# Kernel tuning notes

Measured on AMD Instinct MI355X. Metric: run time of the kernel, lower is better.

The kernel has to match this reference:

```python
import jax, jax.numpy as jnp
import numpy as np

B_J0 = 0.01
BETA = 1.8
GAMMA = 0.5
LENS = 0.5
TAU_M = 20.0
DT = 1.0
IN_SIZE = 4
FULL_LEN = 784
T_STEPS = FULL_LEN // IN_SIZE  # 196 sequential steps
H1, H2, H3 = 512, 512, 512
OUT = 10
BATCH = 256


@jax.custom_vjp
def spike_fn(x):
    # ActFun_adp: heaviside forward, rectangular surrogate backward
    return (x > 0).astype(x.dtype)

def _spike_fwd(x):
    return (x > 0).astype(x.dtype), x

def _spike_bwd(x, g):
    return (GAMMA * g * (jnp.abs(x) < LENS).astype(g.dtype),)

spike_fn.defvjp(_spike_fwd, _spike_bwd)


def _make_mask(dim, c_min, c_max, min_dc, max_dc, phase_max, T=784):
    # Faithful port of create_general_mask
    dc_steps = np.linspace(min_dc, max_dc, dim)
    cycles = np.linspace(c_min, c_max, dim)
    phases = np.linspace(0.0, float(int(phase_max * c_max)), dim)
    rows = []
    for cyc, dc, ph in zip(cycles, dc_steps, phases):
        cyc = int(np.ceil(cyc))
        on = int(np.ceil(dc * cyc))
        pat = [1] * on + [0] * (cyc - on)
        p = int(np.round(ph))
        if p > 0:
            pat = pat[-p:] + pat[:-p]
        rows.append(pat * (T // cyc) + pat[: T % cyc])
    return jnp.asarray(np.array(rows, dtype=np.float32))


def setup_inputs() -> dict:
    key = jax.random.key(0)
    ks = jax.random.split(key, 8)

    def xav(k, o, i):
        return jax.random.normal(k, (o, i), jnp.float32) * np.float32(np.sqrt(2.0 / (o + i)))

    return {
        "x": jax.random.uniform(ks[0], (BATCH, FULL_LEN), jnp.float32),
        "W_i2h1": xav(ks[1], H1, IN_SIZE), "b_i2h1": jnp.zeros(H1, jnp.float32),
        "W_h2h1": xav(ks[2], H1, H1), "b_h2h1": jnp.zeros(H1, jnp.float32),
        "W_i2h2": xav(ks[3], H2, H1), "b_i2h2": jnp.zeros(H2, jnp.float32),
        "W_h2h2": xav(ks[4], H2, H2), "b_h2h2": jnp.zeros(H2, jnp.float32),
        "W_i2h3": xav(ks[5], H3, H2), "b_i2h3": jnp.zeros(H3, jnp.float32),
        "W_h2o": xav(ks[6], OUT, H3), "b_h2o": jnp.zeros(OUT, jnp.float32),
        "tau_adp_h1": jnp.full((H1,), 700.0, jnp.float32),
        "tau_adp_h2": jnp.full((H2,), 700.0, jnp.float32),
        "tau_adp_h3": jnp.full((H3,), 700.0, jnp.float32),
        "mask1": _make_mask(H1, 2, 10, 0.1, 0.9, 0.5),
        "mask2": _make_mask(H2, 2, 10, 0.1, 0.9, 0.5),
        "mask3": _make_mask(H3, 2, 10, 0.1, 0.9, 0.5),
    }


def _forward(x, params, mask1, mask2, mask3):
    (W_i2h1, b_i2h1, W_h2h1, b_h2h1, W_i2h2, b_i2h2, W_h2h2, b_h2h2,
     W_i2h3, b_i2h3, W_h2o, b_h2o, tau1, tau2, tau3) = params
    N = x.shape[0]
    # Faithful to torch: condition uses self.T (196), not 784, so most steps
    # reuse the last IN_SIZE columns.
    cols = np.stack([
        np.arange(s * IN_SIZE, s * IN_SIZE + IN_SIZE)
        if s * IN_SIZE < T_STEPS - IN_SIZE
        else np.arange(FULL_LEN - IN_SIZE, FULL_LEN)
        for s in range(T_STEPS)
    ])
    x_seq = jnp.transpose(x[:, cols], (1, 0, 2))  # (T, N, IN)
    alpha = jnp.exp(jnp.float32(-DT / TAU_M))
    ro1 = jnp.exp(-DT / tau1)
    ro2 = jnp.exp(-DT / tau2)
    ro3 = jnp.exp(-DT / tau3)
    m1_seq = mask1[:, :T_STEPS].T  # (T, H1)
    m2_seq = mask2[:, :T_STEPS].T
    m3_seq = mask3[:, :T_STEPS].T

    def upd(inputs, mem, spk, ro, b, mask):
        # mem_update_NU_adp_skip, isAdapt=1
        b = ro * b + (1.0 - ro) * spk
        Bth = B_J0 + BETA * b
        new_mem = mem * alpha + (1.0 - alpha) * inputs - Bth * spk * DT
        mem = jnp.where(mask == 0, mem, new_mem)
        spk = spike_fn(mem - Bth) * mask
        return mem, spk, b

    def step(carry, xs):
        mem1, s1, bb1, mem2, s2, bb2, mem3, s3, bb3, acc = carry
        x_t, mk1, mk2, mk3 = xs
        h1 = x_t @ W_i2h1.T + b_i2h1 + s1 @ W_h2h1.T + b_h2h1
        mem1, s1, bb1 = upd(h1, mem1, s1, ro1, bb1, mk1)
        h2 = s1 @ W_i2h2.T + b_i2h2 + s2 @ W_h2h2.T + b_h2h2
        mem2, s2, bb2 = upd(h2, mem2, s2, ro2, bb2, mk2)
        h3 = s2 @ W_i2h3.T + b_i2h3
        mem3, s3, bb3 = upd(h3, mem3, s3, ro3, bb3, mk3)
        acc = acc + s3 @ W_h2o.T + b_h2o
        return (mem1, s1, bb1, mem2, s2, bb2, mem3, s3, bb3, acc), None

    z = lambda h: jnp.zeros((N, h), x.dtype)
    bj = lambda h: jnp.full((N, h), B_J0, x.dtype)  # b starts at scalar b_j0
    carry0 = (z(H1), z(H1), bj(H1), z(H2), z(H2), bj(H2), z(H3), z(H3), bj(H3), z(OUT))
    carry, _ = jax.lax.scan(step, carry0, (x_seq, m1_seq, m2_seq, m3_seq))
    return carry[-1] / T_STEPS


def reference(x, W_i2h1, b_i2h1, W_h2h1, b_h2h1, W_i2h2, b_i2h2, W_h2h2, b_h2h2,
              W_i2h3, b_i2h3, W_h2o, b_h2o, tau_adp_h1, tau_adp_h2, tau_adp_h3,
              mask1, mask2, mask3):
    params = (W_i2h1, b_i2h1, W_h2h1, b_h2h1, W_i2h2, b_i2h2, W_h2h2, b_h2h2,
              W_i2h3, b_i2h3, W_h2o, b_h2o, tau_adp_h1, tau_adp_h2, tau_adp_h3)
    return _forward(x, params, mask1, mask2, mask3)
```

## Files before the change

kernel.cpp:

```cpp
#include <hip/hip_runtime.h>

#define H 512
#define TSTEPS 196
#define FLEN 784
#define NBATCH 256

typedef float f4 __attribute__((ext_vector_type(4)));
typedef unsigned long long ull;

#define SLOTB  1050624u
#define SLOTF  262656
#define PADOFF 1048576u
#define MBOFF_F 1050624

__global__ void transpose4(const float* __restrict__ a,
                           const float* __restrict__ b,
                           const float* __restrict__ c,
                           const float* __restrict__ d,
                           float* __restrict__ ws)
{
    __shared__ float tile[32][33];
    const float* src = (blockIdx.z == 0) ? a : (blockIdx.z == 1) ? b
                     : (blockIdx.z == 2) ? c : d;
    float* dst = ws + (size_t)blockIdx.z * SLOTF;
    int bx = blockIdx.x * 32, by = blockIdx.y * 32;
    int tx = threadIdx.x, ty = threadIdx.y;
    for (int r = ty; r < 32; r += 8)
        tile[r][tx] = src[(by + r) * H + bx + tx];
    __syncthreads();
    for (int r = ty; r < 32; r += 8)
        dst[(bx + r) * H + by + tx] = tile[tx][r];
}

__global__ void maskbits(const float* __restrict__ m1, const float* __restrict__ m2,
                         const float* __restrict__ m3, float* __restrict__ ws)
{
    int t = blockIdx.x;
    int z = blockIdx.y;
    int l = threadIdx.x;
    if (z == 3) {
        int idx = t * 64 + l;
        if (idx < 4 * 512) {
            int slot = idx >> 9, pos = idx & 511;
            ws[(size_t)slot * SLOTF + 512 * 512 + pos] = 0.0f;
        }
        return;
    }
    ull* mb = (ull*)(ws + MBOFF_F);
    const float* src = (z == 0) ? m1 : (z == 1) ? m2 : m3;
    for (int w = 0; w < 8; ++w) {
        ull bl = __ballot(src[(w * 64 + l) * FLEN + t] != 0.0f);
        if (l == 0) mb[(size_t)z * (TSTEPS * 8) + t * 8 + w] = bl;
    }
}

__device__ __forceinline__ f4 gsingle(const char* __restrict__ base,
                                      const unsigned* __restrict__ list,
                                      int lo, int hi, unsigned uoff)
{
    f4 a0 = (f4)0.0f, a1 = (f4)0.0f, a2 = (f4)0.0f, a3 = (f4)0.0f;
    for (int i = lo; i < hi; i += 4) {
        unsigned o0 = list[i]     + uoff;
        unsigned o1 = list[i + 1] + uoff;
        unsigned o2 = list[i + 2] + uoff;
        unsigned o3 = list[i + 3] + uoff;
        a0 += *(const f4*)(base + o0);
        a1 += *(const f4*)(base + o1);
        a2 += *(const f4*)(base + o2);
        a3 += *(const f4*)(base + o3);
    }
    return (a0 + a1) + (a2 + a3);
}

__device__ __forceinline__ float sum8(const float* __restrict__ p, int j)
{
    float s0 = p[j] + p[512 + j];
    float s1 = p[1024 + j] + p[1536 + j];
    float s2 = p[2048 + j] + p[2560 + j];
    float s3 = p[3072 + j] + p[3584 + j];
    return (s0 + s1) + (s2 + s3);
}

__device__ __forceinline__ float mbit(const ull* __restrict__ mb, int t, int j)
{
    return ((mb[t * 8 + (j >> 6)] >> (j & 63)) & 1ull) ? 1.0f : 0.0f;
}

__global__ __launch_bounds__(1024)
void lsnn_main(const float* __restrict__ x,
               const float* __restrict__ Wi1,
               const float* __restrict__ bi1, const float* __restrict__ bh1,
               const float* __restrict__ bi2, const float* __restrict__ bh2,
               const float* __restrict__ bi3,
               const float* __restrict__ Wo,  const float* __restrict__ bo,
               const float* __restrict__ tau1, const float* __restrict__ tau2,
               const float* __restrict__ tau3,
               const float* __restrict__ ws,
               float* __restrict__ out)
{
    const char* wsb  = (const char*)ws;
    const char* B_H1 = wsb;
    const char* B_I2 = wsb + SLOTB;
    const char* B_H2 = wsb + 2 * SLOTB;
    const char* B_I3 = wsb + 3 * SLOTB;
    const ull* mb1 = (const ull*)(ws + MBOFF_F);
    const ull* mb2 = mb1 + TSTEPS * 8;
    const ull* mb3 = mb2 + TSTEPS * 8;

    const int n    = blockIdx.x;
    const int tid  = threadIdx.x;
    const int lane = tid & 63;
    const bool lowh = tid < 512;
    const int j    = lowh ? tid : tid - 512;
    const int w8   = (tid >> 6) & 7;
    const int u    = tid & 127;
    const int g    = tid >> 7;
    const unsigned uoff = (unsigned)u << 4;

    __shared__ f4       pU1[8][128], pU2[8][128], pU3[8][128];
    __shared__ unsigned L1[H], L2[H];
    __shared__ ull      ballS[16];

    float4 wi; float bs1, ro1, omr1, mem1, b1, s1;
    float bs2, ro2, omr2, mem2, b2, s2;
    float bs3, ro3, omr3, mem3, b3, s3, cnt3;
    const float alpha = expf(-1.0f / 20.0f);
    const float oma = 1.0f - alpha;
    if (lowh) {
        wi  = reinterpret_cast<const float4*>(Wi1)[j];
        bs1 = bi1[j] + bh1[j];
        ro1 = expf(-1.0f / tau1[j]); omr1 = 1.0f - ro1;
        mem1 = 0.f; b1 = 0.01f; s1 = 0.f;
    } else {
        bs2 = bi2[j] + bh2[j];
        bs3 = bi3[j];
        ro2 = expf(-1.0f / tau2[j]); omr2 = 1.0f - ro2;
        ro3 = expf(-1.0f / tau3[j]); omr3 = 1.0f - ro3;
        mem2 = 0.f; b2 = 0.01f; s2 = 0.f;
        mem3 = 0.f; b3 = 0.01f; s3 = 0.f; cnt3 = 0.f;
    }

    int na1 = 0, na2 = 0, na1p = 0, na2p = 0;
    const float* xr = x + n * FLEN;

    if (tid < 16) ballS[tid] = 0ull;
    __syncthreads();

    for (int t = 0; t <= TSTEPS + 1; ++t) {
        {
            unsigned nib1 = 0, nib2 = 0, nib3 = 0;
            if (t < TSTEPS)
                nib1 = (unsigned)((mb1[t * 8 + (u >> 4)] >> ((u & 15) * 4)) & 0xFull);
            if (t >= 1 && t - 1 < TSTEPS)
                nib2 = (unsigned)((mb2[(t - 1) * 8 + (u >> 4)] >> ((u & 15) * 4)) & 0xFull);
            if (t >= 2)
                nib3 = (unsigned)((mb3[(t - 2) * 8 + (u >> 4)] >> ((u & 15) * 4)) & 0xFull);

            int lo1 = ((na1p * g) >> 3) & ~3, hi1 = ((na1p * (g + 1)) >> 3) & ~3;
            int lo2 = ((na2p * g) >> 3) & ~3, hi2 = ((na2p * (g + 1)) >> 3) & ~3;

            f4 aU1 = (f4)0.0f, aU2 = (f4)0.0f, aU3 = (f4)0.0f;
            if (nib1) aU1 = gsingle(B_H1, L1, lo1, hi1, uoff);
            if (nib2) {
                aU2 = gsingle(B_I2, L1, lo1, hi1, uoff);
                aU2 += gsingle(B_H2, L2, lo2, hi2, uoff);
            }
            if (nib3) aU3 = gsingle(B_I3, L2, lo2, hi2, uoff);
            pU1[g][u] = aU1;
            pU2[g][u] = aU2;
            pU3[g][u] = aU3;
        }
        __syncthreads();

        if (lowh) {
            ull ball = 0;
            if (t < TSTEPS) {
                float mk1 = mbit(mb1, t, j);
                int base = (t < 48) ? (4 * t) : (FLEN - 4);
                float4 xv = *reinterpret_cast<const float4*>(xr + base);
                float h1 = wi.x * xv.x + wi.y * xv.y + wi.z * xv.z + wi.w * xv.w
                         + bs1 + sum8((const float*)&pU1[0][0], j);
                b1 = ro1 * b1 + omr1 * s1;
                float Bth = 0.01f + 1.8f * b1;
                float nm = mem1 * alpha + oma * h1 - Bth * s1;
                mem1 = (mk1 == 0.0f) ? mem1 : nm;
                s1 = (mem1 - Bth > 0.0f) ? mk1 : 0.0f;
                ball = __ballot(s1 != 0.0f);
            }
            if (lane == 0) ballS[w8] = ball;
        } else {
            ull ball = 0;
            int t2 = t - 1;
            if (t2 >= 0 && t2 < TSTEPS) {
                float mk2 = mbit(mb2, t2, j);
                float h2 = bs2 + sum8((const float*)&pU2[0][0], j);
                b2 = ro2 * b2 + omr2 * s2;
                float Bth = 0.01f + 1.8f * b2;
                float nm = mem2 * alpha + oma * h2 - Bth * s2;
                mem2 = (mk2 == 0.0f) ? mem2 : nm;
                s2 = (mem2 - Bth > 0.0f) ? mk2 : 0.0f;
                ball = __ballot(s2 != 0.0f);
            }
            if (lane == 0) ballS[8 + w8] = ball;
            int t3 = t - 2;
            if (t3 >= 0 && t3 < TSTEPS) {
                float mk3 = mbit(mb3, t3, j);
                float h3 = bs3 + sum8((const float*)&pU3[0][0], j);
                b3 = ro3 * b3 + omr3 * s3;
                float Bth = 0.01f + 1.8f * b3;
                float nm = mem3 * alpha + oma * h3 - Bth * s3;
                mem3 = (mk3 == 0.0f) ? mem3 : nm;
                s3 = (mem3 - Bth > 0.0f) ? mk3 : 0.0f;
                cnt3 += s3;
            }
        }
        __syncthreads();

        {
            ull bw[16];
            int c[16];
#pragma unroll
            for (int w = 0; w < 16; ++w) { bw[w] = ballS[w]; c[w] = __popcll(bw[w]); }
            int t1 = 0, t2s = 0;
#pragma unroll
            for (int w = 0; w < 8; ++w) { t1 += c[w]; t2s += c[8 + w]; }
            if (lowh) {
                int pos = 0;
#pragma unroll
                for (int w = 0; w < 8; ++w) if (w < w8) pos += c[w];
                pos += __popcll(bw[w8] & ((1ull << lane) - 1ull));
                if ((bw[w8] >> lane) & 1ull) L1[pos] = (unsigned)j << 11;
            } else {
                int pos = 0;
#pragma unroll
                for (int w = 0; w < 8; ++w) if (w < w8) pos += c[8 + w];
                pos += __popcll(bw[8 + w8] & ((1ull << lane) - 1ull));
                if ((bw[8 + w8] >> lane) & 1ull) L2[pos] = (unsigned)j << 11;
            }
            na1 = t1; na2 = t2s;
            na1p = (na1 + 3) & ~3; na2p = (na2 + 3) & ~3;
            if (tid < 4)      { if (na1 + tid < na1p) L1[na1 + tid] = PADOFF; }
            else if (tid < 8) { int q = tid - 4; if (na2 + q < na2p) L2[na2 + q] = PADOFF; }
        }
        __syncthreads();
    }

    float* c3 = (float*)&pU1[0][0];
    if (!lowh) c3[j] = cnt3;
    __syncthreads();
    int wv = tid >> 6;
    for (int o = wv; o < 10; o += 16) {
        float p = 0.0f;
        for (int i = lane; i < H; i += 64)
            p += Wo[o * H + i] * c3[i];
        for (int off = 32; off > 0; off >>= 1)
            p += __shfl_down(p, off);
        if (lane == 0)
            out[n * 10 + o] = (p + 196.0f * bo[o]) / 196.0f;
    }
}

extern "C" void kernel_launch(void* const* d_in, const int* in_sizes, int n_in,
                              void* d_out, int out_size, void* d_ws, size_t ws_size,
                              hipStream_t stream)
{
    const float* x    = (const float*)d_in[0];
    const float* Wi1  = (const float*)d_in[1];
    const float* bi1  = (const float*)d_in[2];
    const float* Wh1  = (const float*)d_in[3];
    const float* bh1  = (const float*)d_in[4];
    const float* Wi2  = (const float*)d_in[5];
    const float* bi2  = (const float*)d_in[6];
    const float* Wh2  = (const float*)d_in[7];
    const float* bh2  = (const float*)d_in[8];
    const float* Wi3  = (const float*)d_in[9];
    const float* bi3  = (const float*)d_in[10];
    const float* Wo   = (const float*)d_in[11];
    const float* bo   = (const float*)d_in[12];
    const float* tau1 = (const float*)d_in[13];
    const float* tau2 = (const float*)d_in[14];
    const float* tau3 = (const float*)d_in[15];
    const float* m1   = (const float*)d_in[16];
    const float* m2   = (const float*)d_in[17];
    const float* m3   = (const float*)d_in[18];

    float* ws  = (float*)d_ws;
    float* out = (float*)d_out;

    transpose4<<<dim3(16, 16, 4), dim3(32, 8, 1), 0, stream>>>(Wh1, Wi2, Wh2, Wi3, ws);
    maskbits<<<dim3(TSTEPS, 4, 1), 64, 0, stream>>>(m1, m2, m3, ws);

    lsnn_main<<<NBATCH, 1024, 0, stream>>>(x, Wi1, bi1, bh1, bi2, bh2, bi3,
                                           Wo, bo, tau1, tau2, tau3, ws, out);
}
```

Before: 756.7 us.

## Fuse paired sparse gathers sharing spike lists and balance work across groups

Replaces the per-matrix sparse gather with a paired gather that reuses each spike-list offset to load from two weight matrices at once (H1 with I2, H2 with I3). The combined list L1+L2 is split evenly across the eight thread groups, and lists are padded to multiples of 8 and read with vectorized int4 loads. The per-nibble mask skip is removed, so gathers now always run even when mask bits are zero. This trades some wasted loads on masked columns for fewer list reads and better load balance.

Result: faster. 694.8 us (-8.2%).

```diff
diff --git a/kernel.cpp b/kernel.cpp
--- a/kernel.cpp
+++ b/kernel.cpp
@@ -54,22 +54,30 @@
     }
 }
 
-__device__ __forceinline__ f4 gsingle(const char* __restrict__ base,
-                                      const unsigned* __restrict__ list,
-                                      int lo, int hi, unsigned uoff)
-{
-    f4 a0 = (f4)0.0f, a1 = (f4)0.0f, a2 = (f4)0.0f, a3 = (f4)0.0f;
-    for (int i = lo; i < hi; i += 4) {
-        unsigned o0 = list[i]     + uoff;
-        unsigned o1 = list[i + 1] + uoff;
-        unsigned o2 = list[i + 2] + uoff;
-        unsigned o3 = list[i + 3] + uoff;
-        a0 += *(const f4*)(base + o0);
-        a1 += *(const f4*)(base + o1);
-        a2 += *(const f4*)(base + o2);
-        a3 += *(const f4*)(base + o3);
-    }
-    return (a0 + a1) + (a2 + a3);
+__device__ __forceinline__ void gpair8(const char* __restrict__ bA,
+                                       const char* __restrict__ bB,
+                                       const int* __restrict__ list,
+                                       int lo, int hi, unsigned uoff,
+                                       f4& accA, f4& accB)
+{
+    for (int i = lo; i < hi; i += 8) {
+        int4 la = *(const int4*)(list + i);
+        int4 lb = *(const int4*)(list + i + 4);
+        unsigned o0 = (unsigned)la.x + uoff, o1 = (unsigned)la.y + uoff;
+        unsigned o2 = (unsigned)la.z + uoff, o3 = (unsigned)la.w + uoff;
+        unsigned o4 = (unsigned)lb.x + uoff, o5 = (unsigned)lb.y + uoff;
+        unsigned o6 = (unsigned)lb.z + uoff, o7 = (unsigned)lb.w + uoff;
+        f4 va0 = *(const f4*)(bA + o0), vb0 = *(const f4*)(bB + o0);
+        f4 va1 = *(const f4*)(bA + o1), vb1 = *(const f4*)(bB + o1);
+        f4 va2 = *(const f4*)(bA + o2), vb2 = *(const f4*)(bB + o2);
+        f4 va3 = *(const f4*)(bA + o3), vb3 = *(const f4*)(bB + o3);
+        f4 va4 = *(const f4*)(bA + o4), vb4 = *(const f4*)(bB + o4);
+        f4 va5 = *(const f4*)(bA + o5), vb5 = *(const f4*)(bB + o5);
+        f4 va6 = *(const f4*)(bA + o6), vb6 = *(const f4*)(bB + o6);
+        f4 va7 = *(const f4*)(bA + o7), vb7 = *(const f4*)(bB + o7);
+        accA += ((va0 + va1) + (va2 + va3)) + ((va4 + va5) + (va6 + va7));
+        accB += ((vb0 + vb1) + (vb2 + vb3)) + ((vb4 + vb5) + (vb6 + vb7));
+    }
 }
 
 __device__ __forceinline__ float sum8(const float* __restrict__ p, int j)
@@ -117,9 +125,9 @@
     const int g    = tid >> 7;
     const unsigned uoff = (unsigned)u << 4;
 
-    __shared__ f4       pU1[8][128], pU2[8][128], pU3[8][128];
-    __shared__ unsigned L1[H], L2[H];
-    __shared__ ull      ballS[16];
+    __shared__ f4 pU1[8][128], pU2[8][128], pU3[8][128];
+    __shared__ __align__(16) int L1[H], L2[H];
+    __shared__ ull ballS[16];
 
     float4 wi; float bs1, ro1, omr1, mem1, b1, s1;
     float bs2, ro2, omr2, mem2, b2, s2;
@@ -148,24 +156,16 @@
 
     for (int t = 0; t <= TSTEPS + 1; ++t) {
         {
-            unsigned nib1 = 0, nib2 = 0, nib3 = 0;
-            if (t < TSTEPS)
-                nib1 = (unsigned)((mb1[t * 8 + (u >> 4)] >> ((u & 15) * 4)) & 0xFull);
-            if (t >= 1 && t - 1 < TSTEPS)
-                nib2 = (unsigned)((mb2[(t - 1) * 8 + (u >> 4)] >> ((u & 15) * 4)) & 0xFull);
-            if (t >= 2)
-                nib3 = (unsigned)((mb3[(t - 2) * 8 + (u >> 4)] >> ((u & 15) * 4)) & 0xFull);
-
-            int lo1 = ((na1p * g) >> 3) & ~3, hi1 = ((na1p * (g + 1)) >> 3) & ~3;
-            int lo2 = ((na2p * g) >> 3) & ~3, hi2 = ((na2p * (g + 1)) >> 3) & ~3;
-
+            int tot = na1p + na2p;
+            int lo = ((tot * g) >> 3) & ~7, hi = ((tot * (g + 1)) >> 3) & ~7;
+            if (g == 7) hi = tot;
             f4 aU1 = (f4)0.0f, aU2 = (f4)0.0f, aU3 = (f4)0.0f;
-            if (nib1) aU1 = gsingle(B_H1, L1, lo1, hi1, uoff);
-            if (nib2) {
-                aU2 = gsingle(B_I2, L1, lo1, hi1, uoff);
-                aU2 += gsingle(B_H2, L2, lo2, hi2, uoff);
-            }
-            if (nib3) aU3 = gsingle(B_I3, L2, lo2, hi2, uoff);
+            int mi = lo < na1p ? (hi < na1p ? hi : na1p) : na1p;
+            if (lo < mi)
+                gpair8(B_H1, B_I2, L1, lo, mi, uoff, aU1, aU2);
+            int lo2 = (lo > na1p ? lo : na1p) - na1p, hi2 = hi - na1p;
+            if (lo2 < hi2)
+                gpair8(B_H2, B_I3, L2, lo2, hi2, uoff, aU2, aU3);
             pU1[g][u] = aU1;
             pU2[g][u] = aU2;
             pU3[g][u] = aU3;
@@ -229,18 +229,18 @@
 #pragma unroll
                 for (int w = 0; w < 8; ++w) if (w < w8) pos += c[w];
                 pos += __popcll(bw[w8] & ((1ull << lane) - 1ull));
-                if ((bw[w8] >> lane) & 1ull) L1[pos] = (unsigned)j << 11;
+                if ((bw[w8] >> lane) & 1ull) L1[pos] = j << 11;
             } else {
                 int pos = 0;
 #pragma unroll
                 for (int w = 0; w < 8; ++w) if (w < w8) pos += c[8 + w];
                 pos += __popcll(bw[8 + w8] & ((1ull << lane) - 1ull));
-                if ((bw[8 + w8] >> lane) & 1ull) L2[pos] = (unsigned)j << 11;
+                if ((bw[8 + w8] >> lane) & 1ull) L2[pos] = j << 11;
             }
             na1 = t1; na2 = t2s;
-            na1p = (na1 + 3) & ~3; na2p = (na2 + 3) & ~3;
-            if (tid < 4)      { if (na1 + tid < na1p) L1[na1 + tid] = PADOFF; }
-            else if (tid < 8) { int q = tid - 4; if (na2 + q < na2p) L2[na2 + q] = PADOFF; }
+            na1p = (na1 + 7) & ~7; na2p = (na2 + 7) & ~7;
+            if (tid < 8)       { if (na1 + tid < na1p) L1[na1 + tid] = (int)PADOFF; }
+            else if (tid < 16) { int q = tid - 8; if (na2 + q < na2p) L2[na2 + q] = (int)PADOFF; }
         }
         __syncthreads();
     }
```
